# Optimization experiments

Hardware: AMD Instinct MI355X
Metric: run time of the kernel (lower is better)

## Reference

```python
import jax, jax.numpy as jnp
import numpy as np

B = 16; IMG = 127; INC = 64; GROUP = 1; STRIDE = 2; PAD = 1; KS = 3
G = INC // GROUP            # number of ScannCore blocks
S = KS * KS                 # patch_size (attention dim) = 9
SPN = (IMG + 2 * PAD - KS) // STRIDE + 1   # 64
PN = SPN * SPN              # patch_num = 4096
L = GROUP * PN              # sequence length per core


def setup_inputs() -> dict:
    key = jax.random.key(0)
    ks = jax.random.split(key, 9)
    sc = 1.0 / np.sqrt(S)
    x = jax.random.normal(ks[0], (B, INC, IMG, IMG), jnp.float32)
    Wq = jax.random.uniform(ks[1], (G, S, S), jnp.float32, -sc, sc)
    bq = jax.random.uniform(ks[2], (G, S), jnp.float32, -sc, sc)
    Wk = jax.random.uniform(ks[3], (G, S, S), jnp.float32, -sc, sc)
    bk = jax.random.uniform(ks[4], (G, S), jnp.float32, -sc, sc)
    Wv = jax.random.uniform(ks[5], (G, S, S), jnp.float32, -sc, sc)
    bv = jax.random.uniform(ks[6], (G, S), jnp.float32, -sc, sc)
    Wo = jax.random.uniform(ks[7], (G, S, 1), jnp.float32, -sc, sc)
    bo = jax.random.uniform(ks[8], (G, 1), jnp.float32, -sc, sc)
    return dict(x=x, Wq=Wq, bq=bq, Wk=Wk, bk=bk, Wv=Wv, bv=bv, Wo=Wo, bo=bo)


def reference(x, Wq, bq, Wk, bk, Wv, bv, Wo, bo):
    # F.unfold equivalent: [B, INC*S, SPN, SPN] with feature dim ordered (C, kh, kw)
    patches = jax.lax.conv_general_dilated_patches(
        x, (KS, KS), (STRIDE, STRIDE), [(PAD, PAD), (PAD, PAD)])
    t = patches.reshape(B, INC, S, PN)
    # split channels into G groups of GROUP, move patch axis before patch-pixel axis
    t = t.reshape(B, G, GROUP, S, PN).transpose(0, 1, 2, 4, 3).reshape(B, G, L, S)
    # batched tiny single-head attention across all G cores at once
    Q = jnp.einsum('bgls,gst->bglt', t, Wq) + bq[None, :, None, :]
    Km = jnp.einsum('bgls,gst->bglt', t, Wk) + bk[None, :, None, :]
    V = jnp.einsum('bgls,gst->bglt', t, Wv) + bv[None, :, None, :]
    # energy = K^T @ Q over the L axis -> [B, G, S, S]
    energy = jnp.einsum('bgls,bglt->bgst', Km, Q)
    attn = jax.nn.softmax(energy, axis=-1)   # dropout is identity in eval
    # (attn @ V^T)^T -> [B, G, L, S]
    a = jnp.einsum('bgst,bglt->bgls', attn, V)
    out = jnp.einsum('bgls,gso->bglo', a, Wo) + bo[None, :, None, :]  # [B,G,L,1]
    # faithful reshape/permute of original: [B, spn, spn, group] -> [B, group, spn, spn]
    out = out.reshape(B, G, SPN, SPN, GROUP).transpose(0, 1, 4, 2, 3)
    return out.reshape(B, INC, SPN, SPN)
```

## Files before the change

### kernel.cpp

```cpp
#include <hip/hip_runtime.h>
#include <math.h>

#define NB       16
#define IMG      127
#define PLANE    (IMG * IMG)
#define PN       4096
#define PPT      8
#define NROW     (2 * PPT + 1)

#define WS_UC    (1024 * 64)

__device__ __forceinline__ constexpr int symidx(int p, int q) {
    return p * 9 - (p * (p - 1)) / 2 + (q - p);
}

__device__ __forceinline__ float dpp_wave_shr1(float v) {
    return __builtin_bit_cast(float, __builtin_amdgcn_update_dpp(
        0, __builtin_bit_cast(int, v), 0x138, 0xf, 0xf, true));
}

__device__ __forceinline__ float wave_reduce_full(float v) {
#define DPP_ADD(ctrl)                                                          \
    v += __builtin_bit_cast(float, __builtin_amdgcn_update_dpp(                \
             0, __builtin_bit_cast(int, v), (ctrl), 0xf, 0xf, true))
    DPP_ADD(0x111);
    DPP_ADD(0x112);
    DPP_ADD(0x114);
    DPP_ADD(0x118);
    DPP_ADD(0x142);
    DPP_ADD(0x143);
#undef DPP_ADD
    return v;
}

#define XLANE_FENCE() __builtin_amdgcn_wave_barrier()

__global__ void __launch_bounds__(512, 2)
k1_gram(const float* __restrict__ x, float* __restrict__ wsp)
{
    __shared__ float red[8 * 54];

    const int bg  = blockIdx.x;
    const int tid = threadIdx.x;
    const int ow  = tid & 63;
    const int wv  = tid >> 6;
    const int oh0 = wv * PPT;

    const float* __restrict__ xp = x + (size_t)bg * PLANE;
    const bool c2  = (ow < 63);
    const int  ih0 = oh0 * 2 - 1;

    float e0[NROW], e1[NROW];
    #pragma unroll
    for (int r = 0; r < NROW; ++r) {
        const int ih = ih0 + r;
        float a = 0.f, b = 0.f;
        if ((unsigned)ih < (unsigned)IMG) {
            const float* __restrict__ rp = xp + ih * IMG + 2 * ow;
            a = rp[0];
            if (c2) b = rp[1];
        }
        e0[r] = a; e1[r] = b;
    }

    float acc[45], mm[9];
    #pragma unroll
    for (int i = 0; i < 45; ++i) acc[i] = 0.f;
    #pragma unroll
    for (int i = 0; i < 9; ++i)  mm[i] = 0.f;

    #pragma unroll
    for (int k = 0; k < PPT; ++k) {
        float v[9];
        #pragma unroll
        for (int r = 0; r < 3; ++r) {
            const int rr = 2 * k + r;
            v[3 * r + 0] = dpp_wave_shr1(e1[rr]);
            v[3 * r + 1] = e0[rr];
            v[3 * r + 2] = e1[rr];
        }
        int idx = 0;
        #pragma unroll
        for (int p = 0; p < 9; ++p) {
            mm[p] += v[p];
            #pragma unroll
            for (int q = p; q < 9; ++q)
                acc[idx++] += v[p] * v[q];
        }
    }

    #pragma unroll
    for (int i = 0; i < 45; ++i) acc[i] = wave_reduce_full(acc[i]);
    #pragma unroll
    for (int i = 0; i < 9; ++i)  mm[i] = wave_reduce_full(mm[i]);
    if (ow == 63) {
        #pragma unroll
        for (int i = 0; i < 45; ++i) red[wv * 54 + i]      = acc[i];
        #pragma unroll
        for (int i = 0; i < 9; ++i)  red[wv * 54 + 45 + i] = mm[i];
    }
    __syncthreads();

    if (tid < 54) {
        float s = 0.f;
        #pragma unroll
        for (int w = 0; w < 8; ++w) s += red[w * 54 + tid];
        wsp[bg * 64 + tid] = s;
    }
}

__global__ void __launch_bounds__(64, 4)
k2_tiny(const float* __restrict__ wsp, float* __restrict__ wuc,
        const float* __restrict__ Wq, const float* __restrict__ bq,
        const float* __restrict__ Wk, const float* __restrict__ bk,
        const float* __restrict__ Wv, const float* __restrict__ bv,
        const float* __restrict__ Wo, const float* __restrict__ bo)
{
    __shared__ float Msh[45], msh[9], MW[81], en[81], at[81], wt[9];

    const int bg   = blockIdx.x;
    const int g    = bg & 63;
    const int lane = threadIdx.x;

    const float* __restrict__ Wqg = Wq + g * 81;
    const float* __restrict__ Wkg = Wk + g * 81;
    const float* __restrict__ Wvg = Wv + g * 81;

    if (lane < 54) {
        const float s = wsp[bg * 64 + lane];
        if (lane < 45) Msh[lane]      = s;
        else           msh[lane - 45] = s;
    }
    XLANE_FENCE();
    #pragma unroll
    for (int r = 0; r < 2; ++r) {
        const int e = lane + r * 64;
        if (e < 81) {
            const int p = e / 9, t = e % 9;
            float a2 = 0.f;
            #pragma unroll
            for (int q = 0; q < 9; ++q) {
                const int a_ = p < q ? p : q, b_ = p < q ? q : p;
                a2 += Msh[symidx(a_, b_)] * Wqg[q * 9 + t];
            }
            MW[e] = a2;
        }
    }
    XLANE_FENCE();
    #pragma unroll
    for (int r = 0; r < 2; ++r) {
        const int e = lane + r * 64;
        if (e < 81) {
            const int s = e / 9, t = e % 9;
            float km = 0.f, qm = 0.f, a2 = 0.f;
            #pragma unroll
            for (int p = 0; p < 9; ++p) {
                km += Wkg[p * 9 + s] * msh[p];
                qm += Wqg[p * 9 + t] * msh[p];
                a2 += Wkg[p * 9 + s] * MW[p * 9 + t];
            }
            en[e] = a2 + (float)PN * bk[g * 9 + s] * bq[g * 9 + t]
                  + km * bq[g * 9 + t] + bk[g * 9 + s] * qm;
        }
    }
    XLANE_FENCE();
    if (lane < 9) {
        const int s = lane;
        float mx = en[s * 9];
        #pragma unroll
        for (int t = 1; t < 9; ++t) mx = fmaxf(mx, en[s * 9 + t]);
        float ex[9], sum = 0.f;
        #pragma unroll
        for (int t = 0; t < 9; ++t) { ex[t] = expf(en[s * 9 + t] - mx); sum += ex[t]; }
        const float inv = 1.f / sum;
        #pragma unroll
        for (int t = 0; t < 9; ++t) at[s * 9 + t] = ex[t] * inv;
    }
    XLANE_FENCE();
    if (lane < 9) {
        const int t = lane;
        float w = 0.f;
        #pragma unroll
        for (int s = 0; s < 9; ++s) w += at[s * 9 + t] * Wo[g * 9 + s];
        wt[t] = w;
    }
    XLANE_FENCE();
    if (lane < 9) {
        const int p = lane;
        float uu = 0.f;
        #pragma unroll
        for (int t = 0; t < 9; ++t) uu += Wvg[p * 9 + t] * wt[t];
        wuc[bg * 16 + p] = uu;
    }
    if (lane == 12) {
        float cc = bo[g];
        #pragma unroll
        for (int t = 0; t < 9; ++t) cc += bv[g * 9 + t] * wt[t];
        wuc[bg * 16 + 9] = cc;
    }
}

__global__ void __launch_bounds__(512, 4)
k3_out(const float* __restrict__ x, const float* __restrict__ wuc,
       float* __restrict__ out)
{
    const int bg  = blockIdx.x;
    const int tid = threadIdx.x;
    const int ow  = tid & 63;
    const int wv  = tid >> 6;
    const int oh0 = wv * PPT;

    const float* __restrict__ xp = x + (size_t)bg * PLANE;
    const float* __restrict__ up = wuc + bg * 16;

    float ur[9];
    #pragma unroll
    for (int i = 0; i < 9; ++i) ur[i] = up[i];
    const float cc = up[9];

    const bool c2  = (ow < 63);
    const int  ih0 = oh0 * 2 - 1;
    float* __restrict__ op = out + (size_t)bg * PN;

    float a0, b0, a1, b1, a2, b2;
#define LOAD_PAIR(A, B, ihv)                                                   \
    {                                                                          \
        const int ih_ = (ihv);                                                 \
        A = 0.f; B = 0.f;                                                      \
        if ((unsigned)ih_ < (unsigned)IMG) {                                   \
            const float* __restrict__ rp_ = xp + ih_ * IMG + 2 * ow;           \
            A = rp_[0];                                                        \
            if (c2) B = rp_[1];                                                \
        }                                                                      \
    }
    LOAD_PAIR(a0, b0, ih0 + 0);
    LOAD_PAIR(a1, b1, ih0 + 1);
    LOAD_PAIR(a2, b2, ih0 + 2);
    #pragma unroll
    for (int k = 0; k < PPT; ++k) {
        float o = cc;
        o += dpp_wave_shr1(b0) * ur[0]; o += a0 * ur[1]; o += b0 * ur[2];
        o += dpp_wave_shr1(b1) * ur[3]; o += a1 * ur[4]; o += b1 * ur[5];
        o += dpp_wave_shr1(b2) * ur[6]; o += a2 * ur[7]; o += b2 * ur[8];
        op[(oh0 + k) * 64 + ow] = o;
        if (k < PPT - 1) {
            a0 = a2; b0 = b2;
            LOAD_PAIR(a1, b1, ih0 + 2 * k + 3);
            LOAD_PAIR(a2, b2, ih0 + 2 * k + 4);
        }
    }
#undef LOAD_PAIR
}

extern "C" void kernel_launch(void* const* d_in, const int* in_sizes, int n_in,
                              void* d_out, int out_size, void* d_ws, size_t ws_size,
                              hipStream_t stream) {
    (void)in_sizes; (void)n_in; (void)ws_size; (void)out_size;
    const float* x  = (const float*)d_in[0];
    const float* Wq = (const float*)d_in[1];
    const float* bq = (const float*)d_in[2];
    const float* Wk = (const float*)d_in[3];
    const float* bk = (const float*)d_in[4];
    const float* Wv = (const float*)d_in[5];
    const float* bv = (const float*)d_in[6];
    const float* Wo = (const float*)d_in[7];
    const float* bo = (const float*)d_in[8];
    float* out = (float*)d_out;
    float* wsp = (float*)d_ws;
    float* wuc = wsp + WS_UC;

    hipLaunchKernelGGL(k1_gram, dim3(NB * 64), dim3(512), 0, stream, x, wsp);
    hipLaunchKernelGGL(k2_tiny, dim3(NB * 64), dim3(64), 0, stream,
                       wsp, wuc, Wq, bq, Wk, bk, Wv, bv, Wo, bo);
    hipLaunchKernelGGL(k3_out, dim3(NB * 64), dim3(512), 0, stream, x, wuc, out);
}
```

Before: 47.98 us.

## Fuse tiny attention kernel into output kernel and split gram blocks in half

Removes the separate k2_tiny launch. Each k3_out block now reduces the eight per-wave partial Gram sums and computes the 9x9 attention collapse in its first wave before the output pass. k1_gram moves to 2048 blocks of 256 threads, and each wave writes its partial directly to the workspace instead of reducing through shared memory. This saves one launch and a global round trip, and gives k1 more parallelism. The cost is serial tiny-attention work at the start of every k3 block, which makes the other seven waves wait at the barrier.

Measured after the change: 73.58 us. 1.53x slower.

```diff
diff --git a/kernel.cpp b/kernel.cpp
--- a/kernel.cpp
+++ b/kernel.cpp
@@ -8,7 +8,6 @@
 #define PPT      8
 #define NROW     (2 * PPT + 1)
 
-#define WS_UC    (1024 * 64)
 
 __device__ __forceinline__ constexpr int symidx(int p, int q) {
     return p * 9 - (p * (p - 1)) / 2 + (q - p);
@@ -35,16 +34,16 @@
 
 #define XLANE_FENCE() __builtin_amdgcn_wave_barrier()
 
-__global__ void __launch_bounds__(512, 2)
+__global__ void __launch_bounds__(256, 5)
 k1_gram(const float* __restrict__ x, float* __restrict__ wsp)
 {
-    __shared__ float red[8 * 54];
-
-    const int bg  = blockIdx.x;
     const int tid = threadIdx.x;
     const int ow  = tid & 63;
     const int wv  = tid >> 6;
-    const int oh0 = wv * PPT;
+    const int bid = blockIdx.x;
+    const int bg  = bid >> 1;
+    const int oct = ((bid & 1) << 2) | wv;
+    const int oh0 = oct * PPT;
 
     const float* __restrict__ xp = x + (size_t)bg * PLANE;
     const bool c2  = (ow < 63);
@@ -93,131 +92,124 @@
     for (int i = 0; i < 45; ++i) acc[i] = wave_reduce_full(acc[i]);
     #pragma unroll
     for (int i = 0; i < 9; ++i)  mm[i] = wave_reduce_full(mm[i]);
+
     if (ow == 63) {
-        #pragma unroll
-        for (int i = 0; i < 45; ++i) red[wv * 54 + i]      = acc[i];
-        #pragma unroll
-        for (int i = 0; i < 9; ++i)  red[wv * 54 + 45 + i] = mm[i];
-    }
-    __syncthreads();
-
-    if (tid < 54) {
-        float s = 0.f;
-        #pragma unroll
-        for (int w = 0; w < 8; ++w) s += red[w * 54 + tid];
-        wsp[bg * 64 + tid] = s;
-    }
-}
-
-__global__ void __launch_bounds__(64, 4)
-k2_tiny(const float* __restrict__ wsp, float* __restrict__ wuc,
-        const float* __restrict__ Wq, const float* __restrict__ bq,
-        const float* __restrict__ Wk, const float* __restrict__ bk,
-        const float* __restrict__ Wv, const float* __restrict__ bv,
-        const float* __restrict__ Wo, const float* __restrict__ bo)
-{
-    __shared__ float Msh[45], msh[9], MW[81], en[81], at[81], wt[9];
-
-    const int bg   = blockIdx.x;
-    const int g    = bg & 63;
-    const int lane = threadIdx.x;
-
-    const float* __restrict__ Wqg = Wq + g * 81;
-    const float* __restrict__ Wkg = Wk + g * 81;
-    const float* __restrict__ Wvg = Wv + g * 81;
-
-    if (lane < 54) {
-        const float s = wsp[bg * 64 + lane];
-        if (lane < 45) Msh[lane]      = s;
-        else           msh[lane - 45] = s;
-    }
-    XLANE_FENCE();
-    #pragma unroll
-    for (int r = 0; r < 2; ++r) {
-        const int e = lane + r * 64;
-        if (e < 81) {
-            const int p = e / 9, t = e % 9;
-            float a2 = 0.f;
-            #pragma unroll
-            for (int q = 0; q < 9; ++q) {
-                const int a_ = p < q ? p : q, b_ = p < q ? q : p;
-                a2 += Msh[symidx(a_, b_)] * Wqg[q * 9 + t];
-            }
-            MW[e] = a2;
-        }
-    }
-    XLANE_FENCE();
-    #pragma unroll
-    for (int r = 0; r < 2; ++r) {
-        const int e = lane + r * 64;
-        if (e < 81) {
-            const int s = e / 9, t = e % 9;
-            float km = 0.f, qm = 0.f, a2 = 0.f;
-            #pragma unroll
-            for (int p = 0; p < 9; ++p) {
-                km += Wkg[p * 9 + s] * msh[p];
-                qm += Wqg[p * 9 + t] * msh[p];
-                a2 += Wkg[p * 9 + s] * MW[p * 9 + t];
-            }
-            en[e] = a2 + (float)PN * bk[g * 9 + s] * bq[g * 9 + t]
-                  + km * bq[g * 9 + t] + bk[g * 9 + s] * qm;
-        }
-    }
-    XLANE_FENCE();
-    if (lane < 9) {
-        const int s = lane;
-        float mx = en[s * 9];
-        #pragma unroll
-        for (int t = 1; t < 9; ++t) mx = fmaxf(mx, en[s * 9 + t]);
-        float ex[9], sum = 0.f;
-        #pragma unroll
-        for (int t = 0; t < 9; ++t) { ex[t] = expf(en[s * 9 + t] - mx); sum += ex[t]; }
-        const float inv = 1.f / sum;
-        #pragma unroll
-        for (int t = 0; t < 9; ++t) at[s * 9 + t] = ex[t] * inv;
-    }
-    XLANE_FENCE();
-    if (lane < 9) {
-        const int t = lane;
-        float w = 0.f;
-        #pragma unroll
-        for (int s = 0; s < 9; ++s) w += at[s * 9 + t] * Wo[g * 9 + s];
-        wt[t] = w;
-    }
-    XLANE_FENCE();
-    if (lane < 9) {
-        const int p = lane;
-        float uu = 0.f;
-        #pragma unroll
-        for (int t = 0; t < 9; ++t) uu += Wvg[p * 9 + t] * wt[t];
-        wuc[bg * 16 + p] = uu;
-    }
-    if (lane == 12) {
-        float cc = bo[g];
-        #pragma unroll
-        for (int t = 0; t < 9; ++t) cc += bv[g * 9 + t] * wt[t];
-        wuc[bg * 16 + 9] = cc;
+        float* __restrict__ wp = wsp + (size_t)((bg << 3) | oct) * 64;
+        #pragma unroll
+        for (int i = 0; i < 45; ++i) wp[i]      = acc[i];
+        #pragma unroll
+        for (int i = 0; i < 9; ++i)  wp[45 + i] = mm[i];
     }
 }
 
 __global__ void __launch_bounds__(512, 4)
-k3_out(const float* __restrict__ x, const float* __restrict__ wuc,
+k3_out(const float* __restrict__ x, const float* __restrict__ wsp,
+       const float* __restrict__ Wq, const float* __restrict__ bq,
+       const float* __restrict__ Wk, const float* __restrict__ bk,
+       const float* __restrict__ Wv, const float* __restrict__ bv,
+       const float* __restrict__ Wo, const float* __restrict__ bo,
        float* __restrict__ out)
 {
+    __shared__ float Msh[45], msh[9], MW[81], en[81], at[81], wt[9], u_s[9];
+    __shared__ float c_s;
+
     const int bg  = blockIdx.x;
+    const int g   = bg & 63;
     const int tid = threadIdx.x;
     const int ow  = tid & 63;
     const int wv  = tid >> 6;
     const int oh0 = wv * PPT;
 
+    if (tid < 64) {
+        const int lane = tid;
+        const float* __restrict__ Wqg = Wq + g * 81;
+        const float* __restrict__ Wkg = Wk + g * 81;
+        const float* __restrict__ Wvg = Wv + g * 81;
+
+        if (lane < 54) {
+            float s = 0.f;
+            #pragma unroll
+            for (int o = 0; o < 8; ++o)
+                s += wsp[(size_t)((bg << 3) | o) * 64 + lane];
+            if (lane < 45) Msh[lane]      = s;
+            else           msh[lane - 45] = s;
+        }
+        XLANE_FENCE();
+        #pragma unroll
+        for (int r = 0; r < 2; ++r) {
+            const int e = lane + r * 64;
+            if (e < 81) {
+                const int p = e / 9, t = e % 9;
+                float a2 = 0.f;
+                #pragma unroll
+                for (int q = 0; q < 9; ++q) {
+                    const int a_ = p < q ? p : q, b_ = p < q ? q : p;
+                    a2 += Msh[symidx(a_, b_)] * Wqg[q * 9 + t];
+                }
+                MW[e] = a2;
+            }
+        }
+        XLANE_FENCE();
+        #pragma unroll
+        for (int r = 0; r < 2; ++r) {
+            const int e = lane + r * 64;
+            if (e < 81) {
+                const int s = e / 9, t = e % 9;
+                float km = 0.f, qm = 0.f, a2 = 0.f;
+                #pragma unroll
+                for (int p = 0; p < 9; ++p) {
+                    km += Wkg[p * 9 + s] * msh[p];
+                    qm += Wqg[p * 9 + t] * msh[p];
+                    a2 += Wkg[p * 9 + s] * MW[p * 9 + t];
+                }
+                en[e] = a2 + (float)PN * bk[g * 9 + s] * bq[g * 9 + t]
+                      + km * bq[g * 9 + t] + bk[g * 9 + s] * qm;
+            }
+        }
+        XLANE_FENCE();
+        if (lane < 9) {
+            const int s = lane;
+            float mx = en[s * 9];
+            #pragma unroll
+            for (int t = 1; t < 9; ++t) mx = fmaxf(mx, en[s * 9 + t]);
+            float ex[9], sum = 0.f;
+            #pragma unroll
+            for (int t = 0; t < 9; ++t) { ex[t] = expf(en[s * 9 + t] - mx); sum += ex[t]; }
+            const float inv = 1.f / sum;
+            #pragma unroll
+            for (int t = 0; t < 9; ++t) at[s * 9 + t] = ex[t] * inv;
+        }
+        XLANE_FENCE();
+        if (lane < 9) {
+            const int t = lane;
+            float w = 0.f;
+            #pragma unroll
+            for (int s = 0; s < 9; ++s) w += at[s * 9 + t] * Wo[g * 9 + s];
+            wt[t] = w;
+        }
+        XLANE_FENCE();
+        if (lane < 9) {
+            const int p = lane;
+            float uu = 0.f;
+            #pragma unroll
+            for (int t = 0; t < 9; ++t) uu += Wvg[p * 9 + t] * wt[t];
+            u_s[p] = uu;
+        }
+        if (lane == 12) {
+            float cc = bo[g];
+            #pragma unroll
+            for (int t = 0; t < 9; ++t) cc += bv[g * 9 + t] * wt[t];
+            c_s = cc;
+        }
+    }
+    __syncthreads();
+
+    float ur[9];
+    #pragma unroll
+    for (int i = 0; i < 9; ++i) ur[i] = u_s[i];
+    const float cc = c_s;
+
     const float* __restrict__ xp = x + (size_t)bg * PLANE;
-    const float* __restrict__ up = wuc + bg * 16;
-
-    float ur[9];
-    #pragma unroll
-    for (int i = 0; i < 9; ++i) ur[i] = up[i];
-    const float cc = up[9];
-
     const bool c2  = (ow < 63);
     const int  ih0 = oh0 * 2 - 1;
     float* __restrict__ op = out + (size_t)bg * PN;
@@ -267,10 +259,8 @@
     const float* bo = (const float*)d_in[8];
     float* out = (float*)d_out;
     float* wsp = (float*)d_ws;
-    float* wuc = wsp + WS_UC;
-
-    hipLaunchKernelGGL(k1_gram, dim3(NB * 64), dim3(512), 0, stream, x, wsp);
-    hipLaunchKernelGGL(k2_tiny, dim3(NB * 64), dim3(64), 0, stream,
-                       wsp, wuc, Wq, bq, Wk, bk, Wv, bv, Wo, bo);
-    hipLaunchKernelGGL(k3_out, dim3(NB * 64), dim3(512), 0, stream, x, wuc, out);
-}
+
+    hipLaunchKernelGGL(k1_gram, dim3(2048), dim3(256), 0, stream, x, wsp);
+    hipLaunchKernelGGL(k3_out,  dim3(NB * 64), dim3(512), 0, stream,
+                       x, wsp, Wq, bq, Wk, bk, Wv, bv, Wo, bo, out);
+}
```
